# Kernel optimization log

Measured on AMD Instinct MI355X. Metric: run time of the kernel, lower is better.

The kernel has to match this reference:

```python
import jax, jax.numpy as jnp
import numpy as np

B = 65536      # batch
E = 4          # experts per node
F = 32         # per-node input features
H = 256        # hidden width
NODES = 4
D_MID = 128    # intermediate node output dim
D_OUT = 8      # final head dim


def _lin_w(k, fan_in, fan_out):
    b = 1.0 / np.sqrt(fan_in)
    return jax.random.uniform(k, (E, fan_in, fan_out), jnp.float32, -b, b)


def setup_inputs() -> dict:
    key = jax.random.key(0)
    ks = jax.random.split(key, 8)
    feats = jax.random.normal(ks[0], (B, NODES * F), dtype=jnp.float32)
    # routing one-hot blocks embedded in the input vector (as the module expects)
    ohs = [jax.nn.one_hot(jax.random.randint(ks[1 + j], (B,), 0, E), E, dtype=jnp.float32)
           for j in range(NODES)]
    input_val = jnp.concatenate([feats] + ohs, axis=1)  # [B, 144]
    p = {"input_val": input_val}
    kc = iter(jax.random.split(ks[5], 32))
    # node 0: no pre-interface; post: F->H relu, H->D_MID relu
    p["W0_0"] = _lin_w(next(kc), F, H); p["b0_0"] = jnp.full((E, H), 0.1, jnp.float32)
    p["W0_1"] = _lin_w(next(kc), H, D_MID); p["b0_1"] = jnp.full((E, D_MID), 0.1, jnp.float32)
    # nodes 1,2: pre F->H relu; post (D_MID+H)->H relu, H->D_MID relu
    for j in (1, 2):
        p[f"W{j}_pre"] = _lin_w(next(kc), F, H); p[f"b{j}_pre"] = jnp.full((E, H), 0.1, jnp.float32)
        p[f"W{j}_0"] = _lin_w(next(kc), D_MID + H, H); p[f"b{j}_0"] = jnp.full((E, H), 0.1, jnp.float32)
        p[f"W{j}_1"] = _lin_w(next(kc), H, D_MID); p[f"b{j}_1"] = jnp.full((E, D_MID), 0.1, jnp.float32)
    # node 3 (output): pre F->H relu; post (D_MID+H)->H relu, H->D_OUT identity
    p["W3_pre"] = _lin_w(next(kc), F, H); p["b3_pre"] = jnp.full((E, H), 0.1, jnp.float32)
    p["W3_0"] = _lin_w(next(kc), D_MID + H, H); p["b3_0"] = jnp.full((E, H), 0.1, jnp.float32)
    p["W3_1"] = jax.random.uniform(next(kc), (E, H, D_OUT), jnp.float32, -0.003, 0.003)
    p["b3_1"] = jax.random.uniform(next(kc), (E, D_OUT), jnp.float32, -0.003, 0.003)
    return p


def reference(input_val, W0_0, b0_0, W0_1, b0_1,
              W1_pre, b1_pre, W1_0, b1_0, W1_1, b1_1,
              W2_pre, b2_pre, W2_0, b2_0, W2_1, b2_1,
              W3_pre, b3_pre, W3_0, b3_0, W3_1, b3_1):
    relu = jax.nn.relu
    xs = [input_val[:, j * F:(j + 1) * F] for j in range(NODES)]          # per-node features
    ohs = [input_val[:, NODES * F + j * E: NODES * F + (j + 1) * E] for j in range(NODES)]

    def combine(oh, outs):  # oh [B,E] exact one-hot; outs [E,B,D] -> exact per-row expert pick
        return jnp.einsum('be,ebo->bo', oh, outs)

    # node 0 (no previous-level input)
    def n0(W0, b0, W1, b1):
        h = relu(xs[0] @ W0 + b0)
        return relu(h @ W1 + b1)
    x = combine(ohs[0], jax.vmap(n0)(W0_0, b0_0, W0_1, b0_1))  # [B, D_MID]

    def node(xj, xprev, relu_last):
        def f(Wp, bp, W0, b0, W1, b1):
            h = relu(xj @ Wp + bp)                      # pre-interface
            h = jnp.concatenate([xprev, h], axis=-1)    # interface: cat(prev, pre)
            h = relu(h @ W0 + b0)
            o = h @ W1 + b1
            return relu(o) if relu_last else o
        return f

    x = combine(ohs[1], jax.vmap(node(xs[1], x, True))(W1_pre, b1_pre, W1_0, b1_0, W1_1, b1_1))
    x = combine(ohs[2], jax.vmap(node(xs[2], x, True))(W2_pre, b2_pre, W2_0, b2_0, W2_1, b2_1))
    x = combine(ohs[3], jax.vmap(node(xs[3], x, False))(W3_pre, b3_pre, W3_0, b3_0, W3_1, b3_1))
    return x  # [B, D_OUT]
```

## Files before the change

kernel.cpp:

```cpp
#include <hip/hip_runtime.h>
#include <hip/hip_bf16.h>
#include <stdint.h>

typedef unsigned int u32;
typedef unsigned short u16;
typedef unsigned char u8;
typedef __bf16 bf16x8 __attribute__((ext_vector_type(8)));
typedef float f32x4 __attribute__((ext_vector_type(4)));

#define NB 65536
#define NBLK 1280
#define PERM_TOT (NBLK * 64)
#define INVR 0xFFFFFFFFu
#define BLK_DEAD 0xFFFFu

#define O_ROWS 0
#define O_P    256
#define O_H    (O_P + 16384)
#define O_RED  O_P
#define SM_BYTES (O_H + 32768)

__device__ __host__ constexpr int TS(int m) {
  constexpr int t[12] = {0, 64, 320, 384, 1152, 1408, 1472, 2240, 2496, 2560, 3328, 3360};
  return t[m];
}
__device__ const int c_preTS[4]  = {0, 320, 1408, 2496};
__device__ const int c_mainTS[4] = {0, 384, 1472, 2560};
__device__ const int c_outTS[4]  = {64, 1152, 2240, 3328};

struct NodeArgs {
  const float* bpre[4];
  const float* bmain[4];
  const float* bout[4];
};

__device__ __forceinline__ u16 f2bf(float f) {
  u32 u = __builtin_bit_cast(u32, f);
  u32 r = (u + 0x7FFFu + ((u >> 16) & 1u)) >> 16;
  return (u16)r;
}
__device__ __forceinline__ u32 pk2bf(float x, float y) {
  return (u32)f2bf(x) | ((u32)f2bf(y) << 16);
}
__device__ __forceinline__ float relu_f(float x) { return x > 0.f ? x : 0.f; }
__device__ __forceinline__ f32x4 mfma16(bf16x8 a, bf16x8 b, f32x4 c) {
  return __builtin_amdgcn_mfma_f32_16x16x32_bf16(a, b, c, 0, 0, 0);
}

__device__ __forceinline__ void mkpair(f32x4 acc, float bias, bool dorelu, int l16,
                                       u32& w0, u32& w1) {
  float v0 = acc[0] + bias, v1 = acc[1] + bias, v2 = acc[2] + bias, v3 = acc[3] + bias;
  if (dorelu) { v0 = relu_f(v0); v1 = relu_f(v1); v2 = relu_f(v2); v3 = relu_f(v3); }
  u32 a = pk2bf(v0, v1);
  u32 b = pk2bf(v2, v3);
  u32 ax = (u32)__shfl_xor((int)a, 1);
  u32 bx = (u32)__shfl_xor((int)b, 1);
  if ((l16 & 1) == 0) { w0 = (a & 0xffffu) | (ax << 16); w1 = (a >> 16) | (ax & 0xffff0000u); }
  else                { w0 = (bx & 0xffffu) | (b << 16); w1 = (bx >> 16) | (b & 0xffff0000u); }
}

__device__ __forceinline__ void frag_store_pair(char* base, int KT, int m0, int col,
                                                u32 w0, u32 w1) {
  char* d = base + (((m0 >> 4) * KT + (col >> 5)) << 10) +
            (((m0 & 15) + (((col & 31) >> 3) << 4)) << 4) + (col & 7) * 2;
  *(u32*)d = w0; *(u32*)(d + 16) = w1;
}

__device__ __forceinline__ bf16x8 cvt8(float4 a, float4 b) {
  union { u32 w[4]; bf16x8 v; } u;
  u.w[0] = pk2bf(a.x, a.y);
  u.w[1] = pk2bf(a.z, a.w);
  u.w[2] = pk2bf(b.x, b.y);
  u.w[3] = pk2bf(b.z, b.w);
  return u.v;
}


__global__ void k_init(u32* cnt) { cnt[threadIdx.x] = 0u; }

__global__ void k_route(const float* __restrict__ inp, u8* __restrict__ bkt,
                        u32* __restrict__ cnt) {
  __shared__ u32 h[256];
  const int tid = threadIdx.x;
  h[tid] = 0u;
  __syncthreads();
  const int r = blockIdx.x * 256 + tid;
  const float4* oh = (const float4*)(inp + (size_t)r * 144 + 128);
  u32 b = 0;
#pragma unroll
  for (int j = 0; j < 4; j++) {
    float4 v = oh[j];
    u32 e = v.y > 0.5f ? 1u : (v.z > 0.5f ? 2u : (v.w > 0.5f ? 3u : 0u));
    b |= e << (2 * j);
  }
  bkt[r] = (u8)b;
  atomicAdd(&h[b], 1u);
  __syncthreads();
  atomicAdd(&cnt[tid], h[tid]);
}

__global__ void k_scan(const u32* __restrict__ cnt, u32* __restrict__ cur,
                       u16* __restrict__ blk2b, u32* __restrict__ perm) {
  __shared__ u32 s[256];
  const int tid = threadIdx.x;
  const u32 c = cnt[tid];
  const u32 pad = (c + 63u) & ~63u;
  s[tid] = pad;
  __syncthreads();
  for (int d = 1; d < 256; d <<= 1) {
    u32 v = (tid >= d) ? s[tid - d] : 0u;
    __syncthreads();
    s[tid] += v;
    __syncthreads();
  }
  const u32 off = s[tid] - pad;
  const u32 total = s[255];
  cur[tid] = off;
  for (u32 i = off + c; i < off + pad; i++) perm[i] = INVR;
  for (u32 blk = off >> 6; blk < (off + pad) >> 6; blk++) blk2b[blk] = (u16)tid;
  for (u32 i = total + tid; i < PERM_TOT; i += 256) perm[i] = INVR;
  for (u32 blk = (total >> 6) + tid; blk < NBLK; blk += 256) blk2b[blk] = BLK_DEAD;
}

__global__ void k_scatter(const u8* __restrict__ bkt, u32* __restrict__ cur,
                          u32* __restrict__ perm) {
  __shared__ u32 h[256], base[256];
  const int tid = threadIdx.x;
  h[tid] = 0u;
  __syncthreads();
  const int r = blockIdx.x * 256 + tid;
  const u32 b = bkt[r];
  const u32 rank = atomicAdd(&h[b], 1u);
  __syncthreads();
  base[tid] = h[tid] ? atomicAdd(&cur[tid], h[tid]) : 0u;
  __syncthreads();
  perm[base[b] + rank] = (u32)r;
}


struct PrepArgs {
  const float* src[11];
  int K[11], Nsrc[11];
  int tileStart[12];
};

__global__ void k_prep(__bf16* __restrict__ pk, PrepArgs pa) {
  const int tid = threadIdx.x;
  const int gt = blockIdx.x * 4 + (tid >> 6);
  const int lane = tid & 63, quad = lane >> 4, l16 = lane & 15;
  int m = 0;
  while (gt >= pa.tileStart[m + 1]) m++;
  const int loc = gt - pa.tileStart[m];
  const int K = pa.K[m], Ns = pa.Nsrc[m];
  const int Np = Ns < 16 ? 16 : Ns;
  const int KT = K >> 5, NT = Np >> 4;
  const int e = loc / (KT * NT), rem = loc % (KT * NT);
  const int nt = rem / KT, kt = rem % KT;
  const int k = kt * 32 + quad * 8, n = nt * 16 + l16;
  u32 hw[4];
  if (n < Ns) {
    const float* s = pa.src[m] + ((size_t)e * K + k) * Ns + n;
    u16 h[8];
#pragma unroll
    for (int j = 0; j < 8; j++) h[j] = f2bf(s[(size_t)j * Ns]);
    hw[0] = (u32)h[0] | ((u32)h[1] << 16);
    hw[1] = (u32)h[2] | ((u32)h[3] << 16);
    hw[2] = (u32)h[4] | ((u32)h[5] << 16);
    hw[3] = (u32)h[6] | ((u32)h[7] << 16);
  } else {
    hw[0] = hw[1] = hw[2] = hw[3] = 0u;
  }
  uint4 w; w.x = hw[0]; w.y = hw[1]; w.z = hw[2]; w.w = hw[3];
  *(uint4*)((char*)pk + (size_t)gt * 1024 + lane * 16) = w;
}


__global__ __launch_bounds__(256, 3) void fused_k(
    const float* __restrict__ inp, const u32* __restrict__ perm,
    const u16* __restrict__ blk2b, const __bf16* __restrict__ pk,
    NodeArgs na, float* __restrict__ dout) {
  const u32 b = blk2b[blockIdx.x];
  if (b == BLK_DEAD) return;
  __shared__ __align__(16) char sm[SM_BYTES];
  u32* rows = (u32*)sm;
  const int tid = threadIdx.x;
  const int wave = tid >> 6, lane = tid & 63, quad = lane >> 4, l16 = lane & 15;
  if (tid < 64) rows[tid] = perm[blockIdx.x * 64 + tid];
  __syncthreads();
  u32 row_m[4];
#pragma unroll
  for (int mt = 0; mt < 4; mt++) row_m[mt] = rows[mt * 16 + l16];
  const u32 myrow = rows[tid >> 2];

  const int wn0 = wave * 64;
  const int rsel = (quad << 2) + ((l16 & 1) ? 2 : 0);
  const int colp = l16 & ~1;

#pragma clang loop unroll(disable)
  for (int node = 0; node < 4; node++) {
    const u32 e = (b >> (2 * node)) & 3u;
    const __bf16* Wp = pk + (size_t)c_preTS[node] * 512;
    const __bf16* Wm = pk + (size_t)c_mainTS[node] * 512;
    const __bf16* Wo = pk + (size_t)c_outTS[node] * 512;

    bf16x8 xa[4];
#pragma unroll
    for (int mt = 0; mt < 4; mt++) {
      float4 u0 = make_float4(0.f, 0.f, 0.f, 0.f), u1 = u0;
      const u32 r = row_m[mt];
      if (r != INVR) {
        const float4* p = (const float4*)(inp + (size_t)r * 144 + node * 32 + quad * 8);
        u0 = p[0]; u1 = p[1];
      }
      xa[mt] = cvt8(u0, u1);
    }

    __syncthreads();

    {
      float bias[4];
#pragma unroll
      for (int nt = 0; nt < 4; nt++)
        bias[nt] = na.bpre[node][(size_t)e * 256 + wn0 + nt * 16 + l16];
      f32x4 acc[4][4];
#pragma unroll
      for (int i = 0; i < 4; i++)
#pragma unroll
        for (int j = 0; j < 4; j++) acc[i][j] = (f32x4){0.f, 0.f, 0.f, 0.f};
      bf16x8 bw[4];
#pragma unroll
      for (int nt = 0; nt < 4; nt++)
        bw[nt] = *(const bf16x8*)(Wp + (size_t)(e * 16 + (wn0 >> 4) + nt) * 512 + lane * 8);
#pragma unroll
      for (int mt = 0; mt < 4; mt++)
#pragma unroll
        for (int nt = 0; nt < 4; nt++) acc[mt][nt] = mfma16(xa[mt], bw[nt], acc[mt][nt]);
#pragma unroll
      for (int nt = 0; nt < 4; nt++) {
        const int n = wn0 + nt * 16;
#pragma unroll
        for (int mt = 0; mt < 4; mt++) {
          u32 w0, w1;
          mkpair(acc[mt][nt], bias[nt], true, l16, w0, w1);
          frag_store_pair(sm + O_H, 8, mt * 16 + rsel, n + colp, w0, w1);
        }
      }
    }
    __syncthreads();

    if (node > 0) {
      float bias[4];
#pragma unroll
      for (int nt = 0; nt < 4; nt++)
        bias[nt] = na.bmain[node][(size_t)e * 256 + wn0 + nt * 16 + l16];
      f32x4 acc[4][4];
#pragma unroll
      for (int i = 0; i < 4; i++)
#pragma unroll
        for (int j = 0; j < 4; j++) acc[i][j] = (f32x4){0.f, 0.f, 0.f, 0.f};
      const __bf16* bB = Wm + (size_t)(e * 16 + (wn0 >> 4)) * 12 * 512 + lane * 8;
      bf16x8 bb[2][4];
#pragma unroll
      for (int nt = 0; nt < 4; nt++) {
        bb[0][nt] = *(const bf16x8*)(bB + (size_t)(nt * 12 + 0) * 512);
        bb[1][nt] = *(const bf16x8*)(bB + (size_t)(nt * 12 + 1) * 512);
      }
#pragma unroll
      for (int kt = 0; kt < 12; kt++) {
        bf16x8 a[4];
#pragma unroll
        for (int mt = 0; mt < 4; mt++) {
          a[mt] = (kt < 4)
              ? *(const bf16x8*)(sm + O_P + ((mt * 4 + kt) << 10) + lane * 16)
              : *(const bf16x8*)(sm + O_H + ((mt * 8 + (kt - 4)) << 10) + lane * 16);
        }
#pragma unroll
        for (int mt = 0; mt < 4; mt++)
#pragma unroll
          for (int nt = 0; nt < 4; nt++) acc[mt][nt] = mfma16(a[mt], bb[kt & 1][nt], acc[mt][nt]);
        if (kt < 10) {
#pragma unroll
          for (int nt = 0; nt < 4; nt++)
            bb[kt & 1][nt] = *(const bf16x8*)(bB + (size_t)(nt * 12 + kt + 2) * 512);
        }
      }
      __syncthreads();
#pragma unroll
      for (int nt = 0; nt < 4; nt++) {
        const int n = wn0 + nt * 16;
#pragma unroll
        for (int mt = 0; mt < 4; mt++) {
          u32 w0, w1;
          mkpair(acc[mt][nt], bias[nt], true, l16, w0, w1);
          frag_store_pair(sm + O_H, 8, mt * 16 + rsel, n + colp, w0, w1);
        }
      }
      __syncthreads();
    }

    if (node < 3) {
      const int on0 = wave * 32;
      float bias[2];
#pragma unroll
      for (int nt = 0; nt < 2; nt++)
        bias[nt] = na.bout[node][(size_t)e * 128 + on0 + nt * 16 + l16];
      f32x4 acc[4][2];
#pragma unroll
      for (int i = 0; i < 4; i++) { acc[i][0] = (f32x4){0.f,0.f,0.f,0.f}; acc[i][1] = acc[i][0]; }
      const __bf16* bB = Wo + (size_t)(e * 8 + (on0 >> 4)) * 8 * 512 + lane * 8;
      bf16x8 bb[2][2];
#pragma unroll
      for (int nt = 0; nt < 2; nt++) {
        bb[0][nt] = *(const bf16x8*)(bB + (size_t)(nt * 8 + 0) * 512);
        bb[1][nt] = *(const bf16x8*)(bB + (size_t)(nt * 8 + 1) * 512);
      }
#pragma unroll
      for (int kt = 0; kt < 8; kt++) {
        bf16x8 a[4];
#pragma unroll
        for (int mt = 0; mt < 4; mt++)
          a[mt] = *(const bf16x8*)(sm + O_H + ((mt * 8 + kt) << 10) + lane * 16);
#pragma unroll
        for (int mt = 0; mt < 4; mt++)
#pragma unroll
          for (int nt = 0; nt < 2; nt++) acc[mt][nt] = mfma16(a[mt], bb[kt & 1][nt], acc[mt][nt]);
        if (kt < 6) {
#pragma unroll
          for (int nt = 0; nt < 2; nt++)
            bb[kt & 1][nt] = *(const bf16x8*)(bB + (size_t)(nt * 8 + kt + 2) * 512);
        }
      }
#pragma unroll
      for (int nt = 0; nt < 2; nt++) {
        const int n = on0 + nt * 16;
#pragma unroll
        for (int mt = 0; mt < 4; mt++) {
          u32 w0, w1;
          mkpair(acc[mt][nt], bias[nt], true, l16, w0, w1);
          frag_store_pair(sm + O_P, 4, mt * 16 + rsel, n + colp, w0, w1);
        }
      }
    } else {
      f32x4 acc3[4];
#pragma unroll
      for (int i = 0; i < 4; i++) acc3[i] = (f32x4){0.f, 0.f, 0.f, 0.f};
#pragma unroll
      for (int kk = 0; kk < 2; kk++) {
        const int kt = wave * 2 + kk;
        bf16x8 b3 = *(const bf16x8*)(Wo + (size_t)(e * 8 + kt) * 512 + lane * 8);
        bf16x8 a[4];
#pragma unroll
        for (int mt = 0; mt < 4; mt++)
          a[mt] = *(const bf16x8*)(sm + O_H + ((mt * 8 + kt) << 10) + lane * 16);
#pragma unroll
        for (int mt = 0; mt < 4; mt++) acc3[mt] = mfma16(a[mt], b3, acc3[mt]);
      }
#pragma unroll
      for (int mt = 0; mt < 4; mt++)
#pragma unroll
        for (int r = 0; r < 4; r++)
          *(float*)(sm + O_RED +
                    (((size_t)wave * 64 + mt * 16 + quad * 4 + r) * 16 + l16) * 4) = acc3[mt][r];
      __syncthreads();
      const int m = tid >> 2, c = (tid & 3) * 2;
      float s0 = 0.f, s1 = 0.f;
#pragma unroll
      for (int w = 0; w < 4; w++) {
        s0 += *(float*)(sm + O_RED + (((size_t)w * 64 + m) * 16 + c) * 4);
        s1 += *(float*)(sm + O_RED + (((size_t)w * 64 + m) * 16 + c + 1) * 4);
      }
      if (myrow != INVR) {
        float2 o;
        o.x = s0 + na.bout[3][(size_t)e * 8 + c];
        o.y = s1 + na.bout[3][(size_t)e * 8 + c + 1];
        *(float2*)(dout + (size_t)myrow * 8 + c) = o;
      }
    }
  }
}


extern "C" void kernel_launch(void* const* d_in, const int* in_sizes, int n_in,
                              void* d_out, int out_size, void* d_ws, size_t ws_size,
                              hipStream_t stream) {
  (void)in_sizes; (void)n_in; (void)out_size; (void)ws_size;
  const float* inp = (const float*)d_in[0];
  char* ws = (char*)d_ws;

  const size_t oCNT = 0;
  const size_t oCUR = 1024;
  const size_t oBKT = 2048;
  const size_t oB2B = oBKT + NB;
  const size_t oPERM = (oB2B + NBLK * 2 + 255) & ~(size_t)255;
  const size_t oPK = (oPERM + (size_t)PERM_TOT * 4 + 255) & ~(size_t)255;

  u32* cnt = (u32*)(ws + oCNT);
  u32* cur = (u32*)(ws + oCUR);
  u8* bkt = (u8*)(ws + oBKT);
  u16* blk2b = (u16*)(ws + oB2B);
  u32* perm = (u32*)(ws + oPERM);
  __bf16* pk = (__bf16*)(ws + oPK);

  PrepArgs pa;
  const int widx[11] = {1, 3, 5, 7, 9, 11, 13, 15, 17, 19, 21};
  const int Ks[11] = {32, 256, 32, 384, 256, 32, 384, 256, 32, 384, 256};
  const int Ns[11] = {256, 128, 256, 256, 128, 256, 256, 128, 256, 256, 8};
  for (int m = 0; m < 11; m++) {
    pa.src[m] = (const float*)d_in[widx[m]];
    pa.K[m] = Ks[m]; pa.Nsrc[m] = Ns[m]; pa.tileStart[m] = TS(m);
  }
  pa.tileStart[11] = TS(11);

  hipLaunchKernelGGL(k_init, dim3(1), dim3(256), 0, stream, cnt);
  hipLaunchKernelGGL(k_prep, dim3(TS(11) / 4), dim3(256), 0, stream, pk, pa);
  hipLaunchKernelGGL(k_route, dim3(NB / 256), dim3(256), 0, stream, inp, bkt, cnt);
  hipLaunchKernelGGL(k_scan, dim3(1), dim3(256), 0, stream, cnt, cur, blk2b, perm);
  hipLaunchKernelGGL(k_scatter, dim3(NB / 256), dim3(256), 0, stream, bkt, cur, perm);

  NodeArgs na;
  na.bpre[0] = (const float*)d_in[2];
  na.bpre[1] = (const float*)d_in[6];
  na.bpre[2] = (const float*)d_in[12];
  na.bpre[3] = (const float*)d_in[18];
  na.bmain[0] = (const float*)d_in[2];
  na.bmain[1] = (const float*)d_in[8];
  na.bmain[2] = (const float*)d_in[14];
  na.bmain[3] = (const float*)d_in[20];
  na.bout[0] = (const float*)d_in[4];
  na.bout[1] = (const float*)d_in[10];
  na.bout[2] = (const float*)d_in[16];
  na.bout[3] = (const float*)d_in[22];

  fused_k<<<NBLK, 256, 0, stream>>>(inp, perm, blk2b, pk, na, (float*)d_out);
}
```

Baseline: 234.4 us.

## Deterministic per-block histogram routing, deeper weight prefetch, and hardware bf16 conversion

```diff
diff --git a/kernel.cpp b/kernel.cpp
--- a/kernel.cpp
+++ b/kernel.cpp
@@ -34,13 +34,9 @@
   const float* bout[4];
 };
 
-__device__ __forceinline__ u16 f2bf(float f) {
-  u32 u = __builtin_bit_cast(u32, f);
-  u32 r = (u + 0x7FFFu + ((u >> 16) & 1u)) >> 16;
-  return (u16)r;
-}
 __device__ __forceinline__ u32 pk2bf(float x, float y) {
-  return (u32)f2bf(x) | ((u32)f2bf(y) << 16);
+  __hip_bfloat162 h2 = __float22bfloat162_rn(make_float2(x, y));
+  u32 r; __builtin_memcpy(&r, &h2, 4); return r;
 }
 __device__ __forceinline__ float relu_f(float x) { return x > 0.f ? x : 0.f; }
 __device__ __forceinline__ f32x4 mfma16(bf16x8 a, bf16x8 b, f32x4 c) {
@@ -76,10 +72,8 @@
 }
 
 
-__global__ void k_init(u32* cnt) { cnt[threadIdx.x] = 0u; }
-
-__global__ void k_route(const float* __restrict__ inp, u8* __restrict__ bkt,
-                        u32* __restrict__ cnt) {
+__global__ void k_hist(const float* __restrict__ inp, u8* __restrict__ bkt,
+                       u32* __restrict__ hist) {
   __shared__ u32 h[256];
   const int tid = threadIdx.x;
   h[tid] = 0u;
@@ -96,45 +90,45 @@
   bkt[r] = (u8)b;
   atomicAdd(&h[b], 1u);
   __syncthreads();
-  atomicAdd(&cnt[tid], h[tid]);
-}
-
-__global__ void k_scan(const u32* __restrict__ cnt, u32* __restrict__ cur,
+  hist[blockIdx.x * 256 + tid] = h[tid];
+}
+
+__global__ void k_scan(const u32* __restrict__ hist, u32* __restrict__ base,
                        u16* __restrict__ blk2b, u32* __restrict__ perm) {
   __shared__ u32 s[256];
-  const int tid = threadIdx.x;
-  const u32 c = cnt[tid];
+  const int b = threadIdx.x;
+  u32 c = 0;
+  for (int j = 0; j < 256; j++) c += hist[j * 256 + b];
   const u32 pad = (c + 63u) & ~63u;
-  s[tid] = pad;
+  s[b] = pad;
   __syncthreads();
   for (int d = 1; d < 256; d <<= 1) {
-    u32 v = (tid >= d) ? s[tid - d] : 0u;
+    u32 v = (b >= d) ? s[b - d] : 0u;
     __syncthreads();
-    s[tid] += v;
+    s[b] += v;
     __syncthreads();
   }
-  const u32 off = s[tid] - pad;
+  const u32 off = s[b] - pad;
   const u32 total = s[255];
-  cur[tid] = off;
-  for (u32 i = off + c; i < off + pad; i++) perm[i] = INVR;
-  for (u32 blk = off >> 6; blk < (off + pad) >> 6; blk++) blk2b[blk] = (u16)tid;
-  for (u32 i = total + tid; i < PERM_TOT; i += 256) perm[i] = INVR;
-  for (u32 blk = (total >> 6) + tid; blk < NBLK; blk += 256) blk2b[blk] = BLK_DEAD;
-}
-
-__global__ void k_scatter(const u8* __restrict__ bkt, u32* __restrict__ cur,
+  u32 run = off;
+  for (int j = 0; j < 256; j++) { base[j * 256 + b] = run; run += hist[j * 256 + b]; }
+  for (u32 i = run; i < off + pad; i++) perm[i] = INVR;
+  for (u32 blk = off >> 6; blk < (off + pad) >> 6; blk++) blk2b[blk] = (u16)b;
+  for (u32 i = total + b; i < PERM_TOT; i += 256) perm[i] = INVR;
+  for (u32 blk = (total >> 6) + b; blk < NBLK; blk += 256) blk2b[blk] = BLK_DEAD;
+}
+
+__global__ void k_scatter(const u8* __restrict__ bkt, const u32* __restrict__ base,
                           u32* __restrict__ perm) {
-  __shared__ u32 h[256], base[256];
+  __shared__ u32 h[256], bs[256];
   const int tid = threadIdx.x;
   h[tid] = 0u;
+  bs[tid] = base[blockIdx.x * 256 + tid];
   __syncthreads();
   const int r = blockIdx.x * 256 + tid;
   const u32 b = bkt[r];
   const u32 rank = atomicAdd(&h[b], 1u);
-  __syncthreads();
-  base[tid] = h[tid] ? atomicAdd(&cur[tid], h[tid]) : 0u;
-  __syncthreads();
-  perm[base[b] + rank] = (u32)r;
+  perm[bs[b] + rank] = (u32)r;
 }
 
 
@@ -160,13 +154,9 @@
   u32 hw[4];
   if (n < Ns) {
     const float* s = pa.src[m] + ((size_t)e * K + k) * Ns + n;
-    u16 h[8];
-#pragma unroll
-    for (int j = 0; j < 8; j++) h[j] = f2bf(s[(size_t)j * Ns]);
-    hw[0] = (u32)h[0] | ((u32)h[1] << 16);
-    hw[1] = (u32)h[2] | ((u32)h[3] << 16);
-    hw[2] = (u32)h[4] | ((u32)h[5] << 16);
-    hw[3] = (u32)h[6] | ((u32)h[7] << 16);
+#pragma unroll
+    for (int j = 0; j < 4; j++)
+      hw[j] = pk2bf(s[(size_t)(2 * j) * Ns], s[(size_t)(2 * j + 1) * Ns]);
   } else {
     hw[0] = hw[1] = hw[2] = hw[3] = 0u;
   }
@@ -214,57 +204,58 @@
       }
       xa[mt] = cvt8(u0, u1);
     }
+    bf16x8 bw[4];
+    float biasP[4];
+#pragma unroll
+    for (int nt = 0; nt < 4; nt++) {
+      bw[nt] = *(const bf16x8*)(Wp + (size_t)(e * 16 + (wn0 >> 4) + nt) * 512 + lane * 8);
+      biasP[nt] = na.bpre[node][(size_t)e * 256 + wn0 + nt * 16 + l16];
+    }
 
     __syncthreads();
 
-    {
-      float bias[4];
-#pragma unroll
-      for (int nt = 0; nt < 4; nt++)
-        bias[nt] = na.bpre[node][(size_t)e * 256 + wn0 + nt * 16 + l16];
+    f32x4 accp[4][4];
+#pragma unroll
+    for (int i = 0; i < 4; i++)
+#pragma unroll
+      for (int j = 0; j < 4; j++) accp[i][j] = (f32x4){0.f, 0.f, 0.f, 0.f};
+#pragma unroll
+    for (int mt = 0; mt < 4; mt++)
+#pragma unroll
+      for (int nt = 0; nt < 4; nt++) accp[mt][nt] = mfma16(xa[mt], bw[nt], accp[mt][nt]);
+
+    const __bf16* bB = Wm + (size_t)(e * 16 + (wn0 >> 4)) * 12 * 512 + lane * 8;
+    bf16x8 mb[3][4];
+    float biasM[4];
+#pragma unroll
+    for (int nt = 0; nt < 4; nt++) {
+      mb[0][nt] = *(const bf16x8*)(bB + (size_t)(nt * 12 + 0) * 512);
+      mb[1][nt] = *(const bf16x8*)(bB + (size_t)(nt * 12 + 1) * 512);
+      mb[2][nt] = *(const bf16x8*)(bB + (size_t)(nt * 12 + 2) * 512);
+      biasM[nt] = na.bmain[node][(size_t)e * 256 + wn0 + nt * 16 + l16];
+    }
+
+#pragma unroll
+    for (int nt = 0; nt < 4; nt++) {
+      const int n = wn0 + nt * 16;
+#pragma unroll
+      for (int mt = 0; mt < 4; mt++) {
+        u32 w0, w1;
+        mkpair(accp[mt][nt], biasP[nt], true, l16, w0, w1);
+        frag_store_pair(sm + O_H, 8, mt * 16 + rsel, n + colp, w0, w1);
+      }
+    }
+    __syncthreads();
+
+    bf16x8 ob[3][2];
+    float biasO[2];
+
+    if (node > 0) {
       f32x4 acc[4][4];
 #pragma unroll
       for (int i = 0; i < 4; i++)
 #pragma unroll
         for (int j = 0; j < 4; j++) acc[i][j] = (f32x4){0.f, 0.f, 0.f, 0.f};
-      bf16x8 bw[4];
-#pragma unroll
-      for (int nt = 0; nt < 4; nt++)
-        bw[nt] = *(const bf16x8*)(Wp + (size_t)(e * 16 + (wn0 >> 4) + nt) * 512 + lane * 8);
-#pragma unroll
-      for (int mt = 0; mt < 4; mt++)
-#pragma unroll
-        for (int nt = 0; nt < 4; nt++) acc[mt][nt] = mfma16(xa[mt], bw[nt], acc[mt][nt]);
-#pragma unroll
-      for (int nt = 0; nt < 4; nt++) {
-        const int n = wn0 + nt * 16;
-#pragma unroll
-        for (int mt = 0; mt < 4; mt++) {
-          u32 w0, w1;
-          mkpair(acc[mt][nt], bias[nt], true, l16, w0, w1);
-          frag_store_pair(sm + O_H, 8, mt * 16 + rsel, n + colp, w0, w1);
-        }
-      }
-    }
-    __syncthreads();
-
-    if (node > 0) {
-      float bias[4];
-#pragma unroll
-      for (int nt = 0; nt < 4; nt++)
-        bias[nt] = na.bmain[node][(size_t)e * 256 + wn0 + nt * 16 + l16];
-      f32x4 acc[4][4];
-#pragma unroll
-      for (int i = 0; i < 4; i++)
-#pragma unroll
-        for (int j = 0; j < 4; j++) acc[i][j] = (f32x4){0.f, 0.f, 0.f, 0.f};
-      const __bf16* bB = Wm + (size_t)(e * 16 + (wn0 >> 4)) * 12 * 512 + lane * 8;
-      bf16x8 bb[2][4];
-#pragma unroll
-      for (int nt = 0; nt < 4; nt++) {
-        bb[0][nt] = *(const bf16x8*)(bB + (size_t)(nt * 12 + 0) * 512);
-        bb[1][nt] = *(const bf16x8*)(bB + (size_t)(nt * 12 + 1) * 512);
-      }
 #pragma unroll
       for (int kt = 0; kt < 12; kt++) {
         bf16x8 a[4];
@@ -277,43 +268,54 @@
 #pragma unroll
         for (int mt = 0; mt < 4; mt++)
 #pragma unroll
-          for (int nt = 0; nt < 4; nt++) acc[mt][nt] = mfma16(a[mt], bb[kt & 1][nt], acc[mt][nt]);
-        if (kt < 10) {
-#pragma unroll
           for (int nt = 0; nt < 4; nt++)
-            bb[kt & 1][nt] = *(const bf16x8*)(bB + (size_t)(nt * 12 + kt + 2) * 512);
+            acc[mt][nt] = mfma16(a[mt], mb[kt % 3][nt], acc[mt][nt]);
+        if (kt < 9) {
+#pragma unroll
+          for (int nt = 0; nt < 4; nt++)
+            mb[kt % 3][nt] = *(const bf16x8*)(bB + (size_t)(nt * 12 + kt + 3) * 512);
         }
       }
       __syncthreads();
+
+      if (node < 3) {
+        const __bf16* oBp = Wo + (size_t)(e * 8 + ((wave * 32) >> 4)) * 8 * 512 + lane * 8;
+#pragma unroll
+        for (int nt = 0; nt < 2; nt++) {
+          ob[0][nt] = *(const bf16x8*)(oBp + (size_t)(nt * 8 + 0) * 512);
+          ob[1][nt] = *(const bf16x8*)(oBp + (size_t)(nt * 8 + 1) * 512);
+          ob[2][nt] = *(const bf16x8*)(oBp + (size_t)(nt * 8 + 2) * 512);
+          biasO[nt] = na.bout[node][(size_t)e * 128 + wave * 32 + nt * 16 + l16];
+        }
+      }
 #pragma unroll
       for (int nt = 0; nt < 4; nt++) {
         const int n = wn0 + nt * 16;
 #pragma unroll
         for (int mt = 0; mt < 4; mt++) {
           u32 w0, w1;
-          mkpair(acc[mt][nt], bias[nt], true, l16, w0, w1);
+          mkpair(acc[mt][nt], biasM[nt], true, l16, w0, w1);
           frag_store_pair(sm + O_H, 8, mt * 16 + rsel, n + colp, w0, w1);
         }
       }
       __syncthreads();
+    } else {
+      const __bf16* oBp = Wo + (size_t)(e * 8 + ((wave * 32) >> 4)) * 8 * 512 + lane * 8;
+#pragma unroll
+      for (int nt = 0; nt < 2; nt++) {
+        ob[0][nt] = *(const bf16x8*)(oBp + (size_t)(nt * 8 + 0) * 512);
+        ob[1][nt] = *(const bf16x8*)(oBp + (size_t)(nt * 8 + 1) * 512);
+        ob[2][nt] = *(const bf16x8*)(oBp + (size_t)(nt * 8 + 2) * 512);
+        biasO[nt] = na.bout[node][(size_t)e * 128 + wave * 32 + nt * 16 + l16];
+      }
     }
 
     if (node < 3) {
       const int on0 = wave * 32;
-      float bias[2];
-#pragma unroll
-      for (int nt = 0; nt < 2; nt++)
-        bias[nt] = na.bout[node][(size_t)e * 128 + on0 + nt * 16 + l16];
+      const __bf16* oBp = Wo + (size_t)(e * 8 + (on0 >> 4)) * 8 * 512 + lane * 8;
       f32x4 acc[4][2];
 #pragma unroll
       for (int i = 0; i < 4; i++) { acc[i][0] = (f32x4){0.f,0.f,0.f,0.f}; acc[i][1] = acc[i][0]; }
-      const __bf16* bB = Wo + (size_t)(e * 8 + (on0 >> 4)) * 8 * 512 + lane * 8;
-      bf16x8 bb[2][2];
-#pragma unroll
-      for (int nt = 0; nt < 2; nt++) {
-        bb[0][nt] = *(const bf16x8*)(bB + (size_t)(nt * 8 + 0) * 512);
-        bb[1][nt] = *(const bf16x8*)(bB + (size_t)(nt * 8 + 1) * 512);
-      }
 #pragma unroll
       for (int kt = 0; kt < 8; kt++) {
         bf16x8 a[4];
@@ -323,11 +325,12 @@
 #pragma unroll
         for (int mt = 0; mt < 4; mt++)
 #pragma unroll
-          for (int nt = 0; nt < 2; nt++) acc[mt][nt] = mfma16(a[mt], bb[kt & 1][nt], acc[mt][nt]);
-        if (kt < 6) {
-#pragma unroll
           for (int nt = 0; nt < 2; nt++)
-            bb[kt & 1][nt] = *(const bf16x8*)(bB + (size_t)(nt * 8 + kt + 2) * 512);
+            acc[mt][nt] = mfma16(a[mt], ob[kt % 3][nt], acc[mt][nt]);
+        if (kt < 5) {
+#pragma unroll
+          for (int nt = 0; nt < 2; nt++)
+            ob[kt % 3][nt] = *(const bf16x8*)(oBp + (size_t)(nt * 8 + kt + 3) * 512);
         }
       }
 #pragma unroll
@@ -336,7 +339,7 @@
 #pragma unroll
         for (int mt = 0; mt < 4; mt++) {
           u32 w0, w1;
-          mkpair(acc[mt][nt], bias[nt], true, l16, w0, w1);
+          mkpair(acc[mt][nt], biasO[nt], true, l16, w0, w1);
           frag_store_pair(sm + O_P, 4, mt * 16 + rsel, n + colp, w0, w1);
         }
       }
@@ -387,15 +390,15 @@
   const float* inp = (const float*)d_in[0];
   char* ws = (char*)d_ws;
 
-  const size_t oCNT = 0;
-  const size_t oCUR = 1024;
-  const size_t oBKT = 2048;
-  const size_t oB2B = oBKT + NB;
+  const size_t oHIST = 0;
+  const size_t oBASE = oHIST + 65536 * 4;
+  const size_t oBKT  = oBASE + 65536 * 4;
+  const size_t oB2B  = oBKT + NB;
   const size_t oPERM = (oB2B + NBLK * 2 + 255) & ~(size_t)255;
-  const size_t oPK = (oPERM + (size_t)PERM_TOT * 4 + 255) & ~(size_t)255;
-
-  u32* cnt = (u32*)(ws + oCNT);
-  u32* cur = (u32*)(ws + oCUR);
+  const size_t oPK   = (oPERM + (size_t)PERM_TOT * 4 + 255) & ~(size_t)255;
+
+  u32* hist = (u32*)(ws + oHIST);
+  u32* base = (u32*)(ws + oBASE);
   u8* bkt = (u8*)(ws + oBKT);
   u16* blk2b = (u16*)(ws + oB2B);
   u32* perm = (u32*)(ws + oPERM);
@@ -411,11 +414,10 @@
   }
   pa.tileStart[11] = TS(11);
 
-  hipLaunchKernelGGL(k_init, dim3(1), dim3(256), 0, stream, cnt);
   hipLaunchKernelGGL(k_prep, dim3(TS(11) / 4), dim3(256), 0, stream, pk, pa);
-  hipLaunchKernelGGL(k_route, dim3(NB / 256), dim3(256), 0, stream, inp, bkt, cnt);
-  hipLaunchKernelGGL(k_scan, dim3(1), dim3(256), 0, stream, cnt, cur, blk2b, perm);
-  hipLaunchKernelGGL(k_scatter, dim3(NB / 256), dim3(256), 0, stream, bkt, cur, perm);
+  hipLaunchKernelGGL(k_hist, dim3(NB / 256), dim3(256), 0, stream, inp, bkt, hist);
+  hipLaunchKernelGGL(k_scan, dim3(1), dim3(256), 0, stream, hist, base, blk2b, perm);
+  hipLaunchKernelGGL(k_scatter, dim3(NB / 256), dim3(256), 0, stream, bkt, base, perm);
 
   NodeArgs na;
   na.bpre[0] = (const float*)d_in[2];
```

Result: slower. 291.0 us (+24.1%).
